# Kernel optimization log

Measured on AMD Instinct MI355X. Metric: run time of the kernel, lower is better.

The kernel has to match this reference:

```python
import jax, jax.numpy as jnp
import numpy as np

N = 4096       # rows (batch * points)
D = 512        # d_model
H = 8          # num_heads


def setup_inputs() -> dict:
    key = jax.random.key(0)
    ks = jax.random.split(key, 11)
    s = 1.0 / np.sqrt(D).astype(np.float32)
    return {
        "x_q": jax.random.normal(ks[0], (N, D), jnp.float32),
        "x_k": jax.random.normal(ks[1], (N, D), jnp.float32),
        "x_v": jax.random.normal(ks[2], (N, D), jnp.float32),
        "Wq": jax.random.normal(ks[3], (D, D), jnp.float32) * s,
        "bq": jax.random.normal(ks[4], (D,), jnp.float32) * s,
        "Wk": jax.random.normal(ks[5], (D, D), jnp.float32) * s,
        "bk": jax.random.normal(ks[6], (D,), jnp.float32) * s,
        "Wv": jax.random.normal(ks[7], (D, D), jnp.float32) * s,
        "bv": jax.random.normal(ks[8], (D,), jnp.float32) * s,
        "Wo": jax.random.normal(ks[9], (D, D), jnp.float32) * s,
        "bo": jax.random.normal(ks[10], (D,), jnp.float32) * s,
    }


def reference(x_q, x_k, x_v, Wq, bq, Wk, bk, Wv, bv, Wo, bo):
    n, d = x_q.shape
    d_k = d // H
    # linear projections
    q = (x_q @ Wq + bq).reshape(n, H, d_k)  # chunk(dim=-1) == head split
    k = (x_k @ Wk + bk).reshape(n, H, d_k)
    v = (x_v @ Wv + bv).reshape(n, H, d_k)
    # channel-wise outer-product attention: scores[n,h,i,j] = q_i * k_j / sqrt(d_k)
    scale = jnp.asarray(1.0 / np.sqrt(d_k), q.dtype)
    scores = q[..., :, None] * k[..., None, :] * scale  # (n, H, d_k, d_k)
    p = jax.nn.softmax(scores, axis=-1)
    # attn output: p @ v over channel axis -> (n, H, d_k)
    x = jnp.einsum('nhij,nhj->nhi', p, v).reshape(n, d)  # head merge (cat dim=-1)
    return (x_q - x) @ Wo + bo
```

## Files before the change

### kernel.cpp

```cpp
#include <hip/hip_runtime.h>
#include <hip/hip_bf16.h>

#define NROWS 4096
#define DMODEL 512
#define NHEAD 8
#define DKH 64
#define ND (NROWS * DMODEL)
#define DD (DMODEL * DMODEL)

typedef unsigned short u16;
typedef __attribute__((ext_vector_type(8))) short short8;
typedef __attribute__((ext_vector_type(4))) float floatx4;

__device__ __forceinline__ u16 f2b(float f) {
    unsigned u = __float_as_uint(f);
    unsigned r = (u + 0x7fffu + ((u >> 16) & 1u)) >> 16;
    return (u16)r;
}
__device__ __forceinline__ float b2f(u16 v) {
    return __uint_as_float(((unsigned)v) << 16);
}
__device__ __forceinline__ void async16(const void* g, void* l) {
    __builtin_amdgcn_global_load_lds(g, l, 16, 0, 0);
}
__device__ __forceinline__ short8 cvt8(float4 a0, float4 a1) {
    short8 av;
    av[0] = f2b(a0.x); av[1] = f2b(a0.y); av[2] = f2b(a0.z); av[3] = f2b(a0.w);
    av[4] = f2b(a1.x); av[5] = f2b(a1.y); av[6] = f2b(a1.z); av[7] = f2b(a1.w);
    return av;
}

__global__ __launch_bounds__(256) void convert_w(
    const float* __restrict__ W0, const float* __restrict__ W1,
    const float* __restrict__ W2, const float* __restrict__ W3,
    u16* __restrict__ T0, u16* __restrict__ T1, u16* __restrict__ T2,
    u16* __restrict__ T3) {
    __shared__ float tile[32][33];
    int z = blockIdx.z;
    const float* W = z == 0 ? W0 : (z == 1 ? W1 : (z == 2 ? W2 : W3));
    u16* T = z == 0 ? T0 : (z == 1 ? T1 : (z == 2 ? T2 : T3));
    int n0 = blockIdx.x * 32, k0 = blockIdx.y * 32;
    int tx = threadIdx.x, ty = threadIdx.y;
#pragma unroll
    for (int r = 0; r < 32; r += 8)
        tile[ty + r][tx] = W[(size_t)(k0 + ty + r) * DMODEL + n0 + tx];
    __syncthreads();
#pragma unroll
    for (int r = 0; r < 32; r += 8) {
        int n = n0 + ty + r, k = k0 + tx;
        T[(size_t)n * DMODEL + k] = f2b(tile[tx][ty + r]);
    }
}

__global__ __launch_bounds__(256, 2) void proj_attn(
    const float* __restrict__ xq, const float* __restrict__ xk,
    const float* __restrict__ xv, const u16* __restrict__ wtq,
    const u16* __restrict__ wtk, const u16* __restrict__ wtv,
    const float* __restrict__ bq, const float* __restrict__ bk,
    const float* __restrict__ bv, u16* __restrict__ Tb) {
    __shared__ __align__(16) u16 smem[24576];

    const int d = blockIdx.x;
    const int id = (d & 7) * 64 + (d >> 3);
    const int tileM = (id >> 3) * 64;
    const int tileN = (id & 7) * 64;

    const float* XA[3] = {xq, xk, xv};
    const u16* WT[3] = {wtq, wtk, wtv};

    const int tid = threadIdx.x;
    const int wave = tid >> 6, lane = tid & 63;
    const int wm = wave >> 1, wn = wave & 1;
    const int lr4 = lane >> 2, ls = lane & 3;
    const int lrow = lane & 15, sk = lane >> 4;

    const int arow = tid >> 2, aslot = tid & 3;
    const int asw = aslot ^ ((arow >> 1) & 3);
    const float* aptr[3];
#pragma unroll
    for (int m = 0; m < 3; m++)
        aptr[m] = XA[m] + (size_t)(tileM + arow) * 512 + aslot * 8;

    floatx4 acc[3][2][2];
#pragma unroll
    for (int m = 0; m < 3; m++)
#pragma unroll
        for (int i = 0; i < 2; i++)
#pragma unroll
            for (int j = 0; j < 2; j++)
                acc[m][i][j] = (floatx4){0.f, 0.f, 0.f, 0.f};

#pragma unroll
    for (int i = 0; i < 3; i++) {
        int c = wave * 3 + i, m = c >> 2, ch = c & 3;
        int r = ch * 16 + lr4, s = ls ^ ((r >> 1) & 3);
        async16(WT[m] + (size_t)(tileN + r) * 512 + s * 8,
                &smem[12288 + m * 2048 + ch * 512]);
    }
#pragma unroll
    for (int m = 0; m < 3; m++) {
        float4 a0 = *(const float4*)aptr[m];
        float4 a1 = *(const float4*)(aptr[m] + 4);
        *(short8*)&smem[m * 2048 + arow * 32 + asw * 8] = cvt8(a0, a1);
    }
    __syncthreads();

    for (int t = 0; t < 16; ++t) {
        const int cur = t & 1, nxt = cur ^ 1;
        float4 na[3][2];
        if (t < 15) {
#pragma unroll
            for (int m = 0; m < 3; m++) {
                const float* p = aptr[m] + (t + 1) * 32;
                na[m][0] = *(const float4*)p;
                na[m][1] = *(const float4*)(p + 4);
            }
#pragma unroll
            for (int i = 0; i < 3; i++) {
                int c = wave * 3 + i, m = c >> 2, ch = c & 3;
                int r = ch * 16 + lr4, s = ls ^ ((r >> 1) & 3);
                async16(WT[m] + (size_t)(tileN + r) * 512 + (t + 1) * 32 + s * 8,
                        &smem[12288 + (nxt * 3 + m) * 2048 + ch * 512]);
            }
        }
#pragma unroll
        for (int m = 0; m < 3; m++) {
            short8 afr[2], bfr[2];
#pragma unroll
            for (int mi = 0; mi < 2; ++mi) {
                int r = wm * 32 + mi * 16 + lrow;
                int s = sk ^ ((r >> 1) & 3);
                afr[mi] = *(const short8*)&smem[(cur * 3 + m) * 2048 + r * 32 + s * 8];
            }
#pragma unroll
            for (int ni = 0; ni < 2; ++ni) {
                int r = wn * 32 + ni * 16 + lrow;
                int s = sk ^ ((r >> 1) & 3);
                bfr[ni] = *(const short8*)&smem[12288 + (cur * 3 + m) * 2048 + r * 32 + s * 8];
            }
#pragma unroll
            for (int mi = 0; mi < 2; ++mi)
#pragma unroll
                for (int ni = 0; ni < 2; ++ni)
                    acc[m][mi][ni] = __builtin_amdgcn_mfma_f32_16x16x32_bf16(
                        afr[mi], bfr[ni], acc[m][mi][ni], 0, 0, 0);
        }
        if (t < 15) {
#pragma unroll
            for (int m = 0; m < 3; m++)
                *(short8*)&smem[(nxt * 3 + m) * 2048 + arow * 32 + asw * 8] =
                    cvt8(na[m][0], na[m][1]);
        }
        __syncthreads();
    }

    u16* q_ov = smem;
    float* k_ov = (float*)(smem + 4352);
    float* v_ov = (float*)(smem + 13056);
#pragma unroll
    for (int mi = 0; mi < 2; ++mi)
#pragma unroll
        for (int ni = 0; ni < 2; ++ni) {
            int col = wn * 32 + ni * 16 + lrow;
            float bq_ = bq[tileN + col];
            float bk_ = bk[tileN + col];
            float bv_ = bv[tileN + col];
#pragma unroll
            for (int r2 = 0; r2 < 4; r2++) {
                int row = wm * 32 + mi * 16 + sk * 4 + r2;
                q_ov[row * 68 + col] = f2b(acc[0][mi][ni][r2] + bq_);
                k_ov[row * 68 + col] = (acc[1][mi][ni][r2] + bk_) * 0.125f;
                v_ov[row * 68 + col] = acc[2][mi][ni][r2] + bv_;
            }
        }
    __syncthreads();

    for (int i = 0; i < 16; ++i) {
        int nl = wave * 16 + i;
        float qi = b2f(q_ov[nl * 68 + lane]);
        const float* krow = k_ov + nl * 68;
        const float* vrow = v_ov + nl * 68;
        float num = 0.f, den = 0.f;
#pragma unroll
        for (int j = 0; j < 64; j += 4) {
            float4 kv = *(const float4*)(krow + j);
            float4 vv = *(const float4*)(vrow + j);
            float e0 = __expf(qi * kv.x);
            float e1 = __expf(qi * kv.y);
            float e2 = __expf(qi * kv.z);
            float e3 = __expf(qi * kv.w);
            den += e0 + e1 + e2 + e3;
            num += e0 * vv.x + e1 * vv.y + e2 * vv.z + e3 * vv.w;
        }
        size_t gi = (size_t)(tileM + nl) * 512 + tileN + lane;
        Tb[gi] = f2b(xq[gi] - num / den);
    }
}

__global__ __launch_bounds__(256, 2) void out_gemm(const u16* __restrict__ T,
                                                   const u16* __restrict__ wto,
                                                   const float* __restrict__ bo,
                                                   float* __restrict__ C) {
    __shared__ __align__(16) u16 sA[2][2048];
    __shared__ __align__(16) u16 sB[2][2048];
    const int d = blockIdx.x;
    const int id = (d & 7) * 64 + (d >> 3);
    const int tileM = (id >> 3) * 64;
    const int tileN = (id & 7) * 64;

    const int tid = threadIdx.x;
    const int wave = tid >> 6, lane = tid & 63;
    const int wm = wave >> 1, wn = wave & 1;
    const int lr4 = lane >> 2, ls = lane & 3;
    const int lrow = lane & 15, sk = lane >> 4;

    const int r0 = wave * 16 + lr4;
    const int s0 = ls ^ ((r0 >> 1) & 3);
    const u16* aptr = T + (size_t)(tileM + r0) * 512 + s0 * 8;
    const u16* bptr = wto + (size_t)(tileN + r0) * 512 + s0 * 8;

    floatx4 acc[2][2];
#pragma unroll
    for (int i = 0; i < 2; i++)
#pragma unroll
        for (int j = 0; j < 2; j++) acc[i][j] = (floatx4){0.f, 0.f, 0.f, 0.f};

    async16(aptr, &sA[0][wave * 512]);
    async16(bptr, &sB[0][wave * 512]);
    __syncthreads();

    for (int t = 0; t < 16; ++t) {
        const int cur = t & 1, nxt = cur ^ 1;
        if (t < 15) {
            async16(aptr + (t + 1) * 32, &sA[nxt][wave * 512]);
            async16(bptr + (t + 1) * 32, &sB[nxt][wave * 512]);
        }
        short8 afr[2], bfr[2];
#pragma unroll
        for (int mi = 0; mi < 2; ++mi) {
            int r = wm * 32 + mi * 16 + lrow;
            int s = sk ^ ((r >> 1) & 3);
            afr[mi] = *(const short8*)&sA[cur][r * 32 + s * 8];
        }
#pragma unroll
        for (int ni = 0; ni < 2; ++ni) {
            int r = wn * 32 + ni * 16 + lrow;
            int s = sk ^ ((r >> 1) & 3);
            bfr[ni] = *(const short8*)&sB[cur][r * 32 + s * 8];
        }
#pragma unroll
        for (int mi = 0; mi < 2; ++mi)
#pragma unroll
            for (int ni = 0; ni < 2; ++ni)
                acc[mi][ni] = __builtin_amdgcn_mfma_f32_16x16x32_bf16(
                    afr[mi], bfr[ni], acc[mi][ni], 0, 0, 0);
        __syncthreads();
    }

#pragma unroll
    for (int mi = 0; mi < 2; ++mi)
#pragma unroll
        for (int ni = 0; ni < 2; ++ni) {
            int col = tileN + wn * 32 + ni * 16 + lrow;
            float bv = bo[col];
#pragma unroll
            for (int r2 = 0; r2 < 4; r2++) {
                int row = tileM + wm * 32 + mi * 16 + sk * 4 + r2;
                C[(size_t)row * 512 + col] = acc[mi][ni][r2] + bv;
            }
        }
}

extern "C" void kernel_launch(void* const* d_in, const int* in_sizes, int n_in,
                              void* d_out, int out_size, void* d_ws,
                              size_t ws_size, hipStream_t stream) {
    const float* x_q = (const float*)d_in[0];
    const float* x_k = (const float*)d_in[1];
    const float* x_v = (const float*)d_in[2];
    const float* Wq = (const float*)d_in[3];
    const float* bq = (const float*)d_in[4];
    const float* Wk = (const float*)d_in[5];
    const float* bk = (const float*)d_in[6];
    const float* Wv = (const float*)d_in[7];
    const float* bv = (const float*)d_in[8];
    const float* Wo = (const float*)d_in[9];
    const float* bo = (const float*)d_in[10];

    u16* ws = (u16*)d_ws;
    u16* wtq = ws;
    u16* wtk = wtq + DD;
    u16* wtv = wtk + DD;
    u16* wto = wtv + DD;
    u16* Tb = wto + DD;

    convert_w<<<dim3(16, 16, 4), dim3(32, 8), 0, stream>>>(Wq, Wk, Wv, Wo, wtq,
                                                           wtk, wtv, wto);
    proj_attn<<<dim3(512), 256, 0, stream>>>(x_q, x_k, x_v, wtq, wtk, wtv, bq,
                                             bk, bv, Tb);
    out_gemm<<<dim3(512), 256, 0, stream>>>(Tb, wto, bo, (float*)d_out);
}
```

Before: 146.4 us.

## Split fused projection+attention into prep-convert, separate projection GEMM, and attention kernels

Activations are converted to bf16 up front in a combined prep kernel that also transposes the weights. The three projections now run as one GEMM launch of 768 blocks with 64x128 tiles, all operands loaded asynchronously into LDS, writing Q/K/V as bf16 to global memory. A separate attention kernel then reads them back per (row, head). This removes the in-loop fp32-to-bf16 conversion and the heavy fused shared-memory epilogue, and raises occupancy. The cost is extra global round trips for the bf16 activations and Q/K/V, two more kernel launches, and K and V now rounded to bf16 before the attention math.

```diff
diff --git a/kernel.cpp b/kernel.cpp
--- a/kernel.cpp
+++ b/kernel.cpp
@@ -30,43 +30,62 @@
     return av;
 }
 
-__global__ __launch_bounds__(256) void convert_w(
+__global__ __launch_bounds__(256) void prep(
     const float* __restrict__ W0, const float* __restrict__ W1,
     const float* __restrict__ W2, const float* __restrict__ W3,
     u16* __restrict__ T0, u16* __restrict__ T1, u16* __restrict__ T2,
-    u16* __restrict__ T3) {
-    __shared__ float tile[32][33];
-    int z = blockIdx.z;
-    const float* W = z == 0 ? W0 : (z == 1 ? W1 : (z == 2 ? W2 : W3));
-    u16* T = z == 0 ? T0 : (z == 1 ? T1 : (z == 2 ? T2 : T3));
-    int n0 = blockIdx.x * 32, k0 = blockIdx.y * 32;
-    int tx = threadIdx.x, ty = threadIdx.y;
-#pragma unroll
-    for (int r = 0; r < 32; r += 8)
-        tile[ty + r][tx] = W[(size_t)(k0 + ty + r) * DMODEL + n0 + tx];
-    __syncthreads();
-#pragma unroll
-    for (int r = 0; r < 32; r += 8) {
-        int n = n0 + ty + r, k = k0 + tx;
-        T[(size_t)n * DMODEL + k] = f2b(tile[tx][ty + r]);
+    u16* __restrict__ T3, const float* __restrict__ x0,
+    const float* __restrict__ x1, const float* __restrict__ x2,
+    u16* __restrict__ y0, u16* __restrict__ y1, u16* __restrict__ y2) {
+    const int bid = blockIdx.x;
+    const int tid = threadIdx.x;
+    if (bid < 1024) {
+        __shared__ float tile[32][33];
+        int z = bid >> 8, t = bid & 255;
+        const float* W = z == 0 ? W0 : (z == 1 ? W1 : (z == 2 ? W2 : W3));
+        u16* T = z == 0 ? T0 : (z == 1 ? T1 : (z == 2 ? T2 : T3));
+        int n0 = (t & 15) * 32, k0 = (t >> 4) * 32;
+        int tx = tid & 31, ty = tid >> 5;
+#pragma unroll
+        for (int r = 0; r < 32; r += 8)
+            tile[ty + r][tx] = W[(size_t)(k0 + ty + r) * DMODEL + n0 + tx];
+        __syncthreads();
+#pragma unroll
+        for (int r = 0; r < 32; r += 8)
+            T[(size_t)(n0 + ty + r) * DMODEL + k0 + tx] = f2b(tile[tx][ty + r]);
+    } else {
+        int b = bid - 1024;
+        int zz = b >> 10;
+        const float* s = zz == 0 ? x0 : (zz == 1 ? x1 : x2);
+        u16* d = zz == 0 ? y0 : (zz == 1 ? y1 : y2);
+        int i = (b & 1023) * 2048 + tid * 8;
+        float4 a0 = *(const float4*)(s + i);
+        float4 a1 = *(const float4*)(s + i + 4);
+        *(short8*)(d + i) = cvt8(a0, a1);
     }
 }
 
-__global__ __launch_bounds__(256, 2) void proj_attn(
-    const float* __restrict__ xq, const float* __restrict__ xk,
-    const float* __restrict__ xv, const u16* __restrict__ wtq,
+__global__ __launch_bounds__(256, 3) void proj3(
+    const u16* __restrict__ xqb, const u16* __restrict__ xkb,
+    const u16* __restrict__ xvb, const u16* __restrict__ wtq,
     const u16* __restrict__ wtk, const u16* __restrict__ wtv,
     const float* __restrict__ bq, const float* __restrict__ bk,
-    const float* __restrict__ bv, u16* __restrict__ Tb) {
-    __shared__ __align__(16) u16 smem[24576];
+    const float* __restrict__ bv, u16* __restrict__ Q, u16* __restrict__ K,
+    u16* __restrict__ V) {
+    __shared__ __align__(16) u16 sA[2][64 * 32];
+    __shared__ __align__(16) u16 sB[2][128 * 32];
 
     const int d = blockIdx.x;
-    const int id = (d & 7) * 64 + (d >> 3);
-    const int tileM = (id >> 3) * 64;
-    const int tileN = (id & 7) * 64;
-
-    const float* XA[3] = {xq, xk, xv};
-    const u16* WT[3] = {wtq, wtk, wtv};
+    const int id = (d & 7) * 96 + (d >> 3);
+    const int z = id >> 8;
+    const int t2 = id & 255;
+    const int tileM = (t2 >> 2) * 64;
+    const int tileN = (t2 & 3) * 128;
+
+    const u16* A = z == 0 ? xqb : (z == 1 ? xkb : xvb);
+    const u16* Bt = z == 0 ? wtq : (z == 1 ? wtk : wtv);
+    const float* bias = z == 0 ? bq : (z == 1 ? bk : bv);
+    u16* C = z == 0 ? Q : (z == 1 ? K : V);
 
     const int tid = threadIdx.x;
     const int wave = tid >> 6, lane = tid & 63;
@@ -74,127 +93,100 @@
     const int lr4 = lane >> 2, ls = lane & 3;
     const int lrow = lane & 15, sk = lane >> 4;
 
-    const int arow = tid >> 2, aslot = tid & 3;
-    const int asw = aslot ^ ((arow >> 1) & 3);
-    const float* aptr[3];
-#pragma unroll
-    for (int m = 0; m < 3; m++)
-        aptr[m] = XA[m] + (size_t)(tileM + arow) * 512 + aslot * 8;
-
-    floatx4 acc[3][2][2];
-#pragma unroll
-    for (int m = 0; m < 3; m++)
-#pragma unroll
-        for (int i = 0; i < 2; i++)
-#pragma unroll
-            for (int j = 0; j < 2; j++)
-                acc[m][i][j] = (floatx4){0.f, 0.f, 0.f, 0.f};
-
-#pragma unroll
-    for (int i = 0; i < 3; i++) {
-        int c = wave * 3 + i, m = c >> 2, ch = c & 3;
-        int r = ch * 16 + lr4, s = ls ^ ((r >> 1) & 3);
-        async16(WT[m] + (size_t)(tileN + r) * 512 + s * 8,
-                &smem[12288 + m * 2048 + ch * 512]);
-    }
-#pragma unroll
-    for (int m = 0; m < 3; m++) {
-        float4 a0 = *(const float4*)aptr[m];
-        float4 a1 = *(const float4*)(aptr[m] + 4);
-        *(short8*)&smem[m * 2048 + arow * 32 + asw * 8] = cvt8(a0, a1);
-    }
+    const int ra = wave * 16 + lr4;
+    const int sa = ls ^ ((ra >> 1) & 3);
+    const u16* aptr = A + (size_t)(tileM + ra) * 512 + sa * 8;
+    const int rb0 = (wave * 2) * 16 + lr4;
+    const int rb1 = (wave * 2 + 1) * 16 + lr4;
+    const int sb0 = ls ^ ((rb0 >> 1) & 3);
+    const int sb1 = ls ^ ((rb1 >> 1) & 3);
+    const u16* bptr0 = Bt + (size_t)(tileN + rb0) * 512 + sb0 * 8;
+    const u16* bptr1 = Bt + (size_t)(tileN + rb1) * 512 + sb1 * 8;
+
+    floatx4 acc[2][4];
+#pragma unroll
+    for (int i = 0; i < 2; i++)
+#pragma unroll
+        for (int j = 0; j < 4; j++) acc[i][j] = (floatx4){0.f, 0.f, 0.f, 0.f};
+
+    async16(aptr, &sA[0][wave * 512]);
+    async16(bptr0, &sB[0][wave * 1024]);
+    async16(bptr1, &sB[0][wave * 1024 + 512]);
     __syncthreads();
 
     for (int t = 0; t < 16; ++t) {
         const int cur = t & 1, nxt = cur ^ 1;
-        float4 na[3][2];
         if (t < 15) {
-#pragma unroll
-            for (int m = 0; m < 3; m++) {
-                const float* p = aptr[m] + (t + 1) * 32;
-                na[m][0] = *(const float4*)p;
-                na[m][1] = *(const float4*)(p + 4);
-            }
-#pragma unroll
-            for (int i = 0; i < 3; i++) {
-                int c = wave * 3 + i, m = c >> 2, ch = c & 3;
-                int r = ch * 16 + lr4, s = ls ^ ((r >> 1) & 3);
-                async16(WT[m] + (size_t)(tileN + r) * 512 + (t + 1) * 32 + s * 8,
-                        &smem[12288 + (nxt * 3 + m) * 2048 + ch * 512]);
-            }
-        }
-#pragma unroll
-        for (int m = 0; m < 3; m++) {
-            short8 afr[2], bfr[2];
-#pragma unroll
-            for (int mi = 0; mi < 2; ++mi) {
-                int r = wm * 32 + mi * 16 + lrow;
-                int s = sk ^ ((r >> 1) & 3);
-                afr[mi] = *(const short8*)&smem[(cur * 3 + m) * 2048 + r * 32 + s * 8];
-            }
-#pragma unroll
-            for (int ni = 0; ni < 2; ++ni) {
-                int r = wn * 32 + ni * 16 + lrow;
-                int s = sk ^ ((r >> 1) & 3);
-                bfr[ni] = *(const short8*)&smem[12288 + (cur * 3 + m) * 2048 + r * 32 + s * 8];
-            }
-#pragma unroll
-            for (int mi = 0; mi < 2; ++mi)
-#pragma unroll
-                for (int ni = 0; ni < 2; ++ni)
-                    acc[m][mi][ni] = __builtin_amdgcn_mfma_f32_16x16x32_bf16(
-                        afr[mi], bfr[ni], acc[m][mi][ni], 0, 0, 0);
-        }
-        if (t < 15) {
-#pragma unroll
-            for (int m = 0; m < 3; m++)
-                *(short8*)&smem[(nxt * 3 + m) * 2048 + arow * 32 + asw * 8] =
-                    cvt8(na[m][0], na[m][1]);
-        }
+            async16(aptr + (t + 1) * 32, &sA[nxt][wave * 512]);
+            async16(bptr0 + (t + 1) * 32, &sB[nxt][wave * 1024]);
+            async16(bptr1 + (t + 1) * 32, &sB[nxt][wave * 1024 + 512]);
+        }
+        short8 afr[2], bfr[4];
+#pragma unroll
+        for (int mi = 0; mi < 2; ++mi) {
+            int r = wm * 32 + mi * 16 + lrow;
+            int s = sk ^ ((r >> 1) & 3);
+            afr[mi] = *(const short8*)&sA[cur][r * 32 + s * 8];
+        }
+#pragma unroll
+        for (int ni = 0; ni < 4; ++ni) {
+            int r = wn * 64 + ni * 16 + lrow;
+            int s = sk ^ ((r >> 1) & 3);
+            bfr[ni] = *(const short8*)&sB[cur][r * 32 + s * 8];
+        }
+#pragma unroll
+        for (int mi = 0; mi < 2; ++mi)
+#pragma unroll
+            for (int ni = 0; ni < 4; ++ni)
+                acc[mi][ni] = __builtin_amdgcn_mfma_f32_16x16x32_bf16(
+                    afr[mi], bfr[ni], acc[mi][ni], 0, 0, 0);
         __syncthreads();
     }
 
-    u16* q_ov = smem;
-    float* k_ov = (float*)(smem + 4352);
-    float* v_ov = (float*)(smem + 13056);
 #pragma unroll
     for (int mi = 0; mi < 2; ++mi)
 #pragma unroll
-        for (int ni = 0; ni < 2; ++ni) {
-            int col = wn * 32 + ni * 16 + lrow;
-            float bq_ = bq[tileN + col];
-            float bk_ = bk[tileN + col];
-            float bv_ = bv[tileN + col];
+        for (int ni = 0; ni < 4; ++ni) {
+            int col = tileN + wn * 64 + ni * 16 + lrow;
+            float bv_ = bias[col];
 #pragma unroll
             for (int r2 = 0; r2 < 4; r2++) {
-                int row = wm * 32 + mi * 16 + sk * 4 + r2;
-                q_ov[row * 68 + col] = f2b(acc[0][mi][ni][r2] + bq_);
-                k_ov[row * 68 + col] = (acc[1][mi][ni][r2] + bk_) * 0.125f;
-                v_ov[row * 68 + col] = acc[2][mi][ni][r2] + bv_;
+                int row = tileM + wm * 32 + mi * 16 + sk * 4 + r2;
+                C[(size_t)row * 512 + col] = f2b(acc[mi][ni][r2] + bv_);
             }
         }
+}
+
+__global__ __launch_bounds__(256) void attn_kernel(
+    const u16* __restrict__ Qb, const u16* __restrict__ Kb,
+    const u16* __restrict__ Vb, const float* __restrict__ xq,
+    u16* __restrict__ Tout) {
+    __shared__ float lk[4][64];
+    __shared__ float lv[4][64];
+    const int wave = threadIdx.x >> 6, lane = threadIdx.x & 63;
+    const int p = blockIdx.x * 4 + wave;
+    const int n = p >> 3, h = p & 7;
+    const size_t base = (size_t)n * DMODEL + h * DKH;
+
+    float qi = b2f(Qb[base + lane]) * 0.125f;
+    lk[wave][lane] = b2f(Kb[base + lane]);
+    lv[wave][lane] = b2f(Vb[base + lane]);
     __syncthreads();
 
-    for (int i = 0; i < 16; ++i) {
-        int nl = wave * 16 + i;
-        float qi = b2f(q_ov[nl * 68 + lane]);
-        const float* krow = k_ov + nl * 68;
-        const float* vrow = v_ov + nl * 68;
-        float num = 0.f, den = 0.f;
-#pragma unroll
-        for (int j = 0; j < 64; j += 4) {
-            float4 kv = *(const float4*)(krow + j);
-            float4 vv = *(const float4*)(vrow + j);
-            float e0 = __expf(qi * kv.x);
-            float e1 = __expf(qi * kv.y);
-            float e2 = __expf(qi * kv.z);
-            float e3 = __expf(qi * kv.w);
-            den += e0 + e1 + e2 + e3;
-            num += e0 * vv.x + e1 * vv.y + e2 * vv.z + e3 * vv.w;
-        }
-        size_t gi = (size_t)(tileM + nl) * 512 + tileN + lane;
-        Tb[gi] = f2b(xq[gi] - num / den);
+    float num = 0.f, den = 0.f;
+#pragma unroll
+    for (int j = 0; j < 64; j += 4) {
+        float4 kv = *(const float4*)&lk[wave][j];
+        float4 vv = *(const float4*)&lv[wave][j];
+        float e0 = __expf(qi * kv.x);
+        float e1 = __expf(qi * kv.y);
+        float e2 = __expf(qi * kv.z);
+        float e3 = __expf(qi * kv.w);
+        den += e0 + e1 + e2 + e3;
+        num += e0 * vv.x + e1 * vv.y + e2 * vv.z + e3 * vv.w;
     }
+    float t = xq[base + lane] - num / den;
+    Tout[base + lane] = f2b(t);
 }
 
 __global__ __launch_bounds__(256, 2) void out_gemm(const u16* __restrict__ T,
@@ -287,15 +279,23 @@
     const float* bo = (const float*)d_in[10];
 
     u16* ws = (u16*)d_ws;
-    u16* wtq = ws;
+    u16* xqb = ws;
+    u16* xkb = xqb + ND;
+    u16* xvb = xkb + ND;
+    u16* wtq = xvb + ND;
     u16* wtk = wtq + DD;
     u16* wtv = wtk + DD;
     u16* wto = wtv + DD;
-    u16* Tb = wto + DD;
-
-    convert_w<<<dim3(16, 16, 4), dim3(32, 8), 0, stream>>>(Wq, Wk, Wv, Wo, wtq,
-                                                           wtk, wtv, wto);
-    proj_attn<<<dim3(512), 256, 0, stream>>>(x_q, x_k, x_v, wtq, wtk, wtv, bq,
-                                             bk, bv, Tb);
+    u16* Qb = wto + DD;
+    u16* Kb = Qb + ND;
+    u16* Vb = Kb + ND;
+    u16* Tb = Vb + ND;
+
+    prep<<<dim3(4096), 256, 0, stream>>>(Wq, Wk, Wv, Wo, wtq, wtk, wtv, wto,
+                                         x_q, x_k, x_v, xqb, xkb, xvb);
+    proj3<<<dim3(768), 256, 0, stream>>>(xqb, xkb, xvb, wtq, wtk, wtv, bq, bk,
+                                         bv, Qb, Kb, Vb);
+    attn_kernel<<<dim3(NROWS * NHEAD / 4), 256, 0, stream>>>(Qb, Kb, Vb, x_q,
+                                                             Tb);
     out_gemm<<<dim3(512), 256, 0, stream>>>(Tb, wto, bo, (float*)d_out);
 }
```

After: 138.5 us. 5.4% less time.
